# Kernel optimization log

Measured on AMD Instinct MI355X. Metric: run time of the kernel, lower is better.

Reference implementation:

```python
import jax, jax.numpy as jnp
import numpy as np
from jax import lax

WSZ = 8          # window_size
PZ = 8           # pool_size
FILTER_RATE = 0.3


def _gelu(x):
    return jax.nn.gelu(x, approximate=False)  # torch nn.GELU default = exact erf


def setup_inputs() -> dict:
    key = jax.random.key(0)
    ks = jax.random.split(key, 10)
    B, C, H, W = 2, 128, 512, 512
    feature_map = jax.random.normal(ks[0], (B, C, H, W), dtype=jnp.float32)
    uncertain_map = jax.random.uniform(ks[1], (B, H, W), dtype=jnp.float32)
    s = 0.02
    return {
        "feature_map": feature_map,
        "uncertain_map": uncertain_map,
        "q_g_w": jax.random.normal(ks[2], (C, C), dtype=jnp.float32) * s,
        "kv_g_w": jax.random.normal(ks[3], (2 * C, C), dtype=jnp.float32) * s,
        "linner0_w": jax.random.normal(ks[4], (C, C), dtype=jnp.float32) * s,
        "linner0_b": jnp.zeros((C,), dtype=jnp.float32),
        "qkv0_w": jax.random.normal(ks[5], (3 * C, C), dtype=jnp.float32) * s,
        "proj_w": jax.random.normal(ks[6], (C, C), dtype=jnp.float32) * s,
        "proj_b": jnp.zeros((C,), dtype=jnp.float32),
    }


def _forward(feature_map, uncertain_map, q_g_w, kv_g_w, linner0_w, linner0_b,
             qkv0_w, proj_w, proj_b):
    B, C, H, W = feature_map.shape
    wsz, pz = WSZ, PZ
    winsz = wsz * wsz
    nH, nW = H // wsz, W // wsz
    nWin = nH * nW
    scale = (C) ** (-0.5)  # num_heads = 1

    # --- window partition (shift_direct = No_Shift: no padding) ---
    # win_unc: (B, nWin, winsz)
    win_unc = uncertain_map.reshape(B, nH, wsz, nW, wsz).swapaxes(2, 3)
    win_unc = win_unc.reshape(B, nWin, winsz)
    # win_x: (B*nWin, winsz, C)
    win_x = feature_map.transpose(0, 2, 3, 1)  # B,H,W,C
    win_x = win_x.reshape(B, nH, wsz, nW, wsz, C).swapaxes(2, 3)
    win_x = win_x.reshape(B * nWin, winsz, C)

    # --- topk window selection + gather ---
    win_score = win_unc.mean(-1)                 # (B, nWin)
    nWF = int(nWin * FILTER_RATE)
    _, idx = lax.top_k(win_score, nWF)           # (B, nWF)
    flat_idx = (idx + jnp.arange(B, dtype=idx.dtype)[:, None] * nWin).reshape(-1)
    wf = win_x[flat_idx]                         # (B*nWF, winsz, C)

    # --- global branch ---
    # adaptive avg pool (H,W) -> (pz,pz): exact block mean since H%pz==0
    gx = feature_map.reshape(B, C, pz, H // pz, pz, W // pz).mean(axis=(3, 5))
    q = (wf @ q_g_w.T).reshape(B, nWF * winsz, C)
    g = gx.reshape(B, C, pz * pz).swapaxes(1, 2)          # (B, pz*pz, C)
    kv = (g @ kv_g_w.T).reshape(B, pz * pz, 2, C)
    k, v = kv[:, :, 0], kv[:, :, 1]
    attn = jax.nn.softmax(jnp.einsum('bqc,bkc->bqk', q, k) * scale, axis=-1)
    wf = wf + jnp.einsum('bqk,bkc->bqc', attn, v).reshape(B * nWF, winsz, C)

    # --- local branch (local_repeat = 1) ---
    wf = wf + _gelu(wf @ linner0_w.T + linner0_b)
    qkv = (wf @ qkv0_w.T).reshape(B * nWF, winsz, 3, C)
    q, k, v = qkv[:, :, 0], qkv[:, :, 1], qkv[:, :, 2]
    attn = jax.nn.softmax(jnp.einsum('nqc,nkc->nqk', q, k) * scale, axis=-1)
    av = jnp.einsum('nqk,nkc->nqc', attn, v)
    # faithful to torch: (attn@v).transpose(1,2).reshape(n, winsz, C)
    wf = wf + jnp.swapaxes(av, 1, 2).reshape(B * nWF, winsz, C)

    # --- proj ---
    wf = wf + _gelu(wf @ proj_w.T + proj_b)

    # --- scatter back + window merge ---
    win_x = win_x.at[flat_idx].set(wf)
    out = win_x.reshape(B, nH, nW, wsz, wsz, C).swapaxes(2, 3)
    out = out.reshape(B, H, W, C).transpose(0, 3, 1, 2)   # B,C,H,W
    return out


def reference(feature_map, uncertain_map, q_g_w, kv_g_w, linner0_w, linner0_b,
              qkv0_w, proj_w, proj_b):
    return _forward(feature_map, uncertain_map, q_g_w, kv_g_w, linner0_w,
                    linner0_b, qkv0_w, proj_w, proj_b)
```

## Files before the change

kernel.cpp:

```cpp
#include <hip/hip_runtime.h>
#include <math.h>

#define B_    2
#define C_    128
#define H_    512
#define W_    512
#define NWIN  4096
#define NWF   1228
#define NSEL  (B_*NWF)
#define SCALE 0.08838834764831845f

#define WFS   132

__device__ __forceinline__ float wave_max64(float v){
  #pragma unroll
  for (int off = 32; off; off >>= 1) v = fmaxf(v, __shfl_xor(v, off, 64));
  return v;
}
__device__ __forceinline__ float wave_sum64(float v){
  #pragma unroll
  for (int off = 32; off; off >>= 1) v += __shfl_xor(v, off, 64);
  return v;
}
__device__ __forceinline__ float gelu_f(float x){
  return 0.5f * x * (1.0f + erff(x * 0.70710678118654752440f));
}

__global__ void score_k(const float* __restrict__ unc, float* __restrict__ scores){
  int win = blockIdx.x;
  int b = win >> 12, w12 = win & 4095;
  int ih = w12 >> 6, iw = w12 & 63;
  int t = threadIdx.x, r = t >> 3, s = t & 7;
  float v = unc[((size_t)b*512 + ih*8 + r)*512 + iw*8 + s];
  v = wave_sum64(v);
  if (t == 0) scores[win] = v * (1.0f/64.0f);
}

__global__ void select_k(const float* __restrict__ scores, int* __restrict__ sel){
  int b = blockIdx.x;
  __shared__ float s[NWIN];
  for (int i = threadIdx.x; i < NWIN; i += 1024) s[i] = scores[b*NWIN + i];
  __syncthreads();
  for (int w = threadIdx.x; w < NWIN; w += 1024){
    float mys = s[w];
    int rank = 0;
    for (int j2 = 0; j2 < NWIN; ++j2){
      float o = s[j2];
      rank += (o > mys) || (o == mys && j2 < w);
    }
    if (rank < NWF) sel[b*NWF + rank] = w;
  }
}

__global__ void pool_k(const float* __restrict__ fm, float* __restrict__ g){
  int id = blockIdx.x;
  int p = id & 63, c = (id >> 6) & 127, b = id >> 13;
  int i = p >> 3, k = p & 7;
  const float* base = fm + (((size_t)b*128 + c)*512 + i*64)*512 + k*64;
  int tid = threadIdx.x;
  float sum = 0.0f;
  #pragma unroll
  for (int it = 0; it < 16; ++it){
    int f = it*256 + tid;
    int j2 = f >> 6, l = f & 63;
    sum += base[(size_t)j2*512 + l];
  }
  __shared__ float red[256];
  red[tid] = sum; __syncthreads();
  for (int s2 = 128; s2; s2 >>= 1){
    if (tid < s2) red[tid] += red[tid + s2];
    __syncthreads();
  }
  if (tid == 0) g[((b*64 + p) << 7) + c] = red[0] * (1.0f/4096.0f);
}

__global__ void kv_k(const float* __restrict__ g, const float* __restrict__ kvw,
                     float* __restrict__ kbuf, float* __restrict__ vbp){
  int gid = blockIdx.x*256 + threadIdx.x;
  int c = gid & 127, p = (gid >> 7) & 63, b = gid >> 13;
  const float* grow = g + ((b*64 + p) << 7);
  const float* wk = kvw + (c << 7);
  const float* wv = kvw + ((128 + c) << 7);
  float ka = 0.0f, va = 0.0f;
  #pragma unroll 8
  for (int d = 0; d < 128; ++d){ float gv = grow[d]; ka += gv*wk[d]; va += gv*wv[d]; }
  kbuf[gid] = ka;
  vbp[((((b*16 + (p >> 2))*128 + c)) << 2) + (p & 3)] = va;
}

__global__ void mb_k(const float* __restrict__ kbuf, const float* __restrict__ qgw,
                     float* __restrict__ mbp){
  int gid = blockIdx.x*256 + threadIdx.x;
  int d = gid & 127, p = (gid >> 7) & 63, b = gid >> 13;
  const float* krow = kbuf + ((b*64 + p) << 7);
  float acc = 0.0f;
  #pragma unroll 8
  for (int c = 0; c < 128; ++c) acc += krow[c] * qgw[(c << 7) + d];
  mbp[((((b*32 + (d >> 2))*64 + p)) << 2) + (d & 3)] = acc;
}

__global__ void m2p_k(const float* __restrict__ qkvw, float* __restrict__ m2p){
  int gid = blockIdx.x*256 + threadIdx.x;
  int e = gid & 127, dq = gid >> 7;
  float ax = 0.f, ay = 0.f, az = 0.f, aw = 0.f;
  for (int c = 0; c < 128; ++c){
    float kv2 = qkvw[((128 + c) << 7) + e];
    const float4 q4 = *(const float4*)(qkvw + (c << 7) + dq*4);
    ax += q4.x*kv2; ay += q4.y*kv2; az += q4.z*kv2; aw += q4.w*kv2;
  }
  ((float4*)m2p)[dq*128 + e] = make_float4(ax, ay, az, aw);
}

__global__ void pack_k(const float* __restrict__ l0w, const float* __restrict__ pw,
                       const float* __restrict__ qkvw,
                       float* __restrict__ l0wp, float* __restrict__ pwp,
                       float* __restrict__ wv2p){
  int gid = blockIdx.x*256 + threadIdx.x;
  int c = gid & 127, dq = gid >> 7;
  ((float4*)l0wp)[dq*128 + c] = *(const float4*)(l0w + (c << 7) + dq*4);
  ((float4*)pwp )[dq*128 + c] = *(const float4*)(pw  + (c << 7) + dq*4);
  ((float4*)wv2p)[dq*128 + c] = *(const float4*)(qkvw + ((256 + c) << 7) + dq*4);
}

__global__ __launch_bounds__(256, 2) void mega_k(
    const float* __restrict__ fm, const int* __restrict__ sel,
    const float* __restrict__ mbp, const float* __restrict__ vbp,
    const float* __restrict__ m2p, const float* __restrict__ wv2p,
    const float* __restrict__ l0wp, const float* __restrict__ l0b,
    const float* __restrict__ pwp,  const float* __restrict__ pb,
    float* __restrict__ out)
{
  __shared__ float wf_s[64*WFS];
  __shared__ float aux_s[64*128];
  const int tid = threadIdx.x, lane = tid & 63, wv = tid >> 6;
  const int ci = tid & 127, hi = tid >> 7;
  const int j = blockIdx.x;
  const int b = j / NWF;
  const int win = sel[j];
  const int ih = win >> 6, iw = win & 63;

  {
    const float* fmb = fm + ((size_t)b*128)*512*512;
    #pragma unroll
    for (int it = 0; it < 8; ++it){
      int idx = it*256 + tid;
      int c = idx >> 4, rem = idx & 15, r = rem >> 1, q = rem & 1;
      float4 v = *(const float4*)(fmb + ((size_t)c*512 + ih*8 + r)*512 + iw*8 + q*4);
      int t0 = r*8 + q*4;
      wf_s[(t0+0)*WFS + c] = v.x;
      wf_s[(t0+1)*WFS + c] = v.y;
      wf_s[(t0+2)*WFS + c] = v.z;
      wf_s[(t0+3)*WFS + c] = v.w;
    }
  }
  __syncthreads();

  {
    const float4* mb4 = (const float4*)mbp + (size_t)b*2048 + lane;
    float acc[16];
    #pragma unroll
    for (int r2 = 0; r2 < 16; ++r2) acc[r2] = 0.f;
    const float* wrow = wf_s + (wv*16)*WFS;
    float4 m = mb4[0];
    for (int dq = 0; dq < 32; ++dq){
      int nq = (dq + 1 < 32) ? dq + 1 : 31;
      float4 mn = mb4[nq*64];
      #pragma unroll
      for (int r2 = 0; r2 < 16; ++r2){
        float4 x = *(const float4*)(wrow + r2*WFS + dq*4);
        acc[r2] += x.x*m.x + x.y*m.y + x.z*m.z + x.w*m.w;
      }
      m = mn;
    }
    #pragma unroll
    for (int r2 = 0; r2 < 16; ++r2){
      float a = acc[r2] * SCALE;
      float mx = wave_max64(a);
      float e = __expf(a - mx);
      float p = e / wave_sum64(e);
      aux_s[(wv*16 + r2)*128 + lane] = p;
    }
  }
  __syncthreads();

  {
    const float4* v4p = (const float4*)vbp + (size_t)b*2048 + ci;
    float acc[32];
    #pragma unroll
    for (int jj = 0; jj < 32; ++jj) acc[jj] = 0.f;
    float4 v = v4p[0];
    for (int pq = 0; pq < 16; ++pq){
      int nq = (pq + 1 < 16) ? pq + 1 : 15;
      float4 vn = v4p[nq*128];
      #pragma unroll
      for (int jj = 0; jj < 32; ++jj){
        float4 p4 = *(const float4*)(aux_s + (2*jj + hi)*128 + pq*4);
        acc[jj] += p4.x*v.x + p4.y*v.y + p4.z*v.z + p4.w*v.w;
      }
      v = vn;
    }
    #pragma unroll
    for (int jj = 0; jj < 32; ++jj) wf_s[(2*jj + hi)*WFS + ci] += acc[jj];
  }
  __syncthreads();

  {
    const float4* w4 = (const float4*)l0wp + ci;
    float bias = l0b[ci];
    float acc[32];
    #pragma unroll
    for (int jj = 0; jj < 32; ++jj) acc[jj] = bias;
    float4 w = w4[0];
    for (int dq = 0; dq < 32; ++dq){
      int nq = (dq + 1 < 32) ? dq + 1 : 31;
      float4 wn = w4[nq*128];
      #pragma unroll
      for (int jj = 0; jj < 32; ++jj){
        float4 x = *(const float4*)(wf_s + (2*jj + hi)*WFS + dq*4);
        acc[jj] += x.x*w.x + x.y*w.y + x.z*w.z + x.w*w.w;
      }
      w = wn;
    }
    __syncthreads();
    #pragma unroll
    for (int jj = 0; jj < 32; ++jj)
      wf_s[(2*jj + hi)*WFS + ci] += gelu_f(acc[jj]);
  }
  __syncthreads();

  {
    const float4* w4 = (const float4*)m2p + ci;
    float acc[32];
    #pragma unroll
    for (int jj = 0; jj < 32; ++jj) acc[jj] = 0.f;
    float4 w = w4[0];
    for (int dq = 0; dq < 32; ++dq){
      int nq = (dq + 1 < 32) ? dq + 1 : 31;
      float4 wn = w4[nq*128];
      #pragma unroll
      for (int jj = 0; jj < 32; ++jj){
        float4 x = *(const float4*)(wf_s + (2*jj + hi)*WFS + dq*4);
        acc[jj] += x.x*w.x + x.y*w.y + x.z*w.z + x.w*w.w;
      }
      w = wn;
    }
    #pragma unroll
    for (int jj = 0; jj < 32; ++jj) aux_s[(2*jj + hi)*128 + ci] = acc[jj];
  }
  __syncthreads();

  {
    float acc[16];
    #pragma unroll
    for (int r2 = 0; r2 < 16; ++r2) acc[r2] = 0.f;
    const float* trow = aux_s + (wv*16)*128;
    for (int eq = 0; eq < 32; ++eq){
      float4 wr = *(const float4*)(wf_s + lane*WFS + eq*4);
      #pragma unroll
      for (int r2 = 0; r2 < 16; ++r2){
        float4 t4 = *(const float4*)(trow + r2*128 + eq*4);
        acc[r2] += t4.x*wr.x + t4.y*wr.y + t4.z*wr.z + t4.w*wr.w;
      }
    }
    #pragma unroll
    for (int r2 = 0; r2 < 16; ++r2){
      float a = acc[r2] * SCALE;
      float mx = wave_max64(a);
      float e = __expf(a - mx);
      float p = e / wave_sum64(e);
      aux_s[(wv*16 + r2)*128 + lane] = p;
    }
  }
  __syncthreads();

  {
    float acc[32];
    #pragma unroll
    for (int jj = 0; jj < 32; ++jj) acc[jj] = 0.f;
    for (int tq = 0; tq < 16; ++tq){
      float w0 = wf_s[(4*tq + 0)*WFS + ci];
      float w1 = wf_s[(4*tq + 1)*WFS + ci];
      float w2 = wf_s[(4*tq + 2)*WFS + ci];
      float w3 = wf_s[(4*tq + 3)*WFS + ci];
      #pragma unroll
      for (int jj = 0; jj < 32; ++jj){
        float4 p4 = *(const float4*)(aux_s + (2*jj + hi)*128 + tq*4);
        acc[jj] += p4.x*w0 + p4.y*w1 + p4.z*w2 + p4.w*w3;
      }
    }
    __syncthreads();
    #pragma unroll
    for (int jj = 0; jj < 32; ++jj) aux_s[(2*jj + hi)*128 + ci] = acc[jj];
  }
  __syncthreads();

  {
    const float4* w4 = (const float4*)wv2p + ci;
    float acc[32];
    #pragma unroll
    for (int jj = 0; jj < 32; ++jj) acc[jj] = 0.f;
    float4 w = w4[0];
    for (int dq = 0; dq < 32; ++dq){
      int nq = (dq + 1 < 32) ? dq + 1 : 31;
      float4 wn = w4[nq*128];
      #pragma unroll
      for (int jj = 0; jj < 32; ++jj){
        float4 u4 = *(const float4*)(aux_s + (2*jj + hi)*128 + dq*4);
        acc[jj] += u4.x*w.x + u4.y*w.y + u4.z*w.z + u4.w*w.w;
      }
      w = wn;
    }
    int row = ci >> 1, cbase = (ci & 1)*64 + hi;
    #pragma unroll
    for (int jj = 0; jj < 32; ++jj)
      wf_s[row*WFS + cbase + 2*jj] += acc[jj];
  }
  __syncthreads();

  {
    const float4* w4 = (const float4*)pwp + ci;
    float bias = pb[ci];
    float acc[32];
    #pragma unroll
    for (int jj = 0; jj < 32; ++jj) acc[jj] = bias;
    float4 w = w4[0];
    for (int dq = 0; dq < 32; ++dq){
      int nq = (dq + 1 < 32) ? dq + 1 : 31;
      float4 wn = w4[nq*128];
      #pragma unroll
      for (int jj = 0; jj < 32; ++jj){
        float4 x = *(const float4*)(wf_s + (2*jj + hi)*WFS + dq*4);
        acc[jj] += x.x*w.x + x.y*w.y + x.z*w.z + x.w*w.w;
      }
      w = wn;
    }
    __syncthreads();
    #pragma unroll
    for (int jj = 0; jj < 32; ++jj)
      wf_s[(2*jj + hi)*WFS + ci] += gelu_f(acc[jj]);
  }
  __syncthreads();

  {
    float* outb = out + ((size_t)b*128)*512*512;
    #pragma unroll
    for (int it = 0; it < 8; ++it){
      int idx = it*256 + tid;
      int c = idx >> 4, rem = idx & 15, r = rem >> 1, q = rem & 1;
      int t0 = r*8 + q*4;
      float4 v;
      v.x = wf_s[(t0+0)*WFS + c];
      v.y = wf_s[(t0+1)*WFS + c];
      v.z = wf_s[(t0+2)*WFS + c];
      v.w = wf_s[(t0+3)*WFS + c];
      *(float4*)(outb + ((size_t)c*512 + ih*8 + r)*512 + iw*8 + q*4) = v;
    }
  }
}

extern "C" void kernel_launch(void* const* d_in, const int* in_sizes, int n_in,
                              void* d_out, int out_size, void* d_ws, size_t ws_size,
                              hipStream_t stream) {
  const float* fm   = (const float*)d_in[0];
  const float* unc  = (const float*)d_in[1];
  const float* qgw  = (const float*)d_in[2];
  const float* kvw  = (const float*)d_in[3];
  const float* l0w  = (const float*)d_in[4];
  const float* l0b  = (const float*)d_in[5];
  const float* qkvw = (const float*)d_in[6];
  const float* pw   = (const float*)d_in[7];
  const float* pb   = (const float*)d_in[8];
  float* out = (float*)d_out;

  float* ws     = (float*)d_ws;
  float* scores = ws;
  int*   sel    = (int*)(ws + 8192);
  float* g      = ws + 12288;
  float* mbp    = ws + 12288;
  float* kbuf   = ws + 28672;
  float* wv2p   = ws + 28672;
  float* vbp    = ws + 45056;
  float* m2p    = ws + 61440;
  float* l0wp   = ws + 77824;
  float* pwp    = ws + 94208;

  hipMemcpyAsync(out, fm, (size_t)B_*C_*H_*W_*sizeof(float),
                 hipMemcpyDeviceToDevice, stream);

  score_k <<<B_*NWIN, 64, 0, stream>>>(unc, scores);
  select_k<<<B_, 1024, 0, stream>>>(scores, sel);
  pool_k  <<<B_*C_*64, 256, 0, stream>>>(fm, g);
  kv_k    <<<64, 256, 0, stream>>>(g, kvw, kbuf, vbp);
  mb_k    <<<64, 256, 0, stream>>>(kbuf, qgw, mbp);
  m2p_k   <<<16, 256, 0, stream>>>(qkvw, m2p);
  pack_k  <<<16, 256, 0, stream>>>(l0w, pw, qkvw, l0wp, pwp, wv2p);
  mega_k  <<<NSEL, 256, 0, stream>>>(fm, sel, mbp, vbp, m2p, wv2p,
                                     l0wp, l0b, pwp, pb, out);
}
```

Baseline: 2.069 ms.

## Fuse output copy into pool kernel and remap mega_k to row-per-wave work

The separate device-to-device copy of the feature map into the output is removed, and pool_k now writes each float4 it reads to the output, so the 268MB tensor is read once instead of twice. In mega_k each wave now owns 16 token rows and computes both 64-column halves, so several stages only depend on rows the wave itself produced and most __syncthreads barriers are dropped. Accumulations are split into sequential per-element adds. The risks are higher register pressure from the two 16-wide accumulator sets and correctness depending on the reduced barriers being sufficient.

```diff
diff --git a/kernel.cpp b/kernel.cpp
--- a/kernel.cpp
+++ b/kernel.cpp
@@ -52,18 +52,23 @@
   }
 }
 
-__global__ void pool_k(const float* __restrict__ fm, float* __restrict__ g){
+__global__ void pool_k(const float* __restrict__ fm, float* __restrict__ g,
+                       float* __restrict__ out){
   int id = blockIdx.x;
   int p = id & 63, c = (id >> 6) & 127, b = id >> 13;
   int i = p >> 3, k = p & 7;
-  const float* base = fm + (((size_t)b*128 + c)*512 + i*64)*512 + k*64;
+  size_t off = (((size_t)b*128 + c)*512 + i*64)*512 + k*64;
+  const float* base = fm + off;
+  float* ob = out + off;
   int tid = threadIdx.x;
   float sum = 0.0f;
   #pragma unroll
-  for (int it = 0; it < 16; ++it){
-    int f = it*256 + tid;
-    int j2 = f >> 6, l = f & 63;
-    sum += base[(size_t)j2*512 + l];
+  for (int it = 0; it < 4; ++it){
+    int idx = it*256 + tid;
+    int j2 = idx >> 4, l = (idx & 15)*4;
+    float4 v = *(const float4*)(base + (size_t)j2*512 + l);
+    *(float4*)(ob + (size_t)j2*512 + l) = v;
+    sum += v.x + v.y + v.z + v.w;
   }
   __shared__ float red[256];
   red[tid] = sum; __syncthreads();
@@ -133,7 +138,7 @@
   __shared__ float wf_s[64*WFS];
   __shared__ float aux_s[64*128];
   const int tid = threadIdx.x, lane = tid & 63, wv = tid >> 6;
-  const int ci = tid & 127, hi = tid >> 7;
+  const int r0 = wv*16;
   const int j = blockIdx.x;
   const int b = j / NWF;
   const int win = sel[j];
@@ -159,185 +164,204 @@
     const float4* mb4 = (const float4*)mbp + (size_t)b*2048 + lane;
     float acc[16];
     #pragma unroll
-    for (int r2 = 0; r2 < 16; ++r2) acc[r2] = 0.f;
-    const float* wrow = wf_s + (wv*16)*WFS;
+    for (int k = 0; k < 16; ++k) acc[k] = 0.f;
+    const float* wrow = wf_s + r0*WFS;
     float4 m = mb4[0];
     for (int dq = 0; dq < 32; ++dq){
       int nq = (dq + 1 < 32) ? dq + 1 : 31;
       float4 mn = mb4[nq*64];
       #pragma unroll
-      for (int r2 = 0; r2 < 16; ++r2){
-        float4 x = *(const float4*)(wrow + r2*WFS + dq*4);
-        acc[r2] += x.x*m.x + x.y*m.y + x.z*m.z + x.w*m.w;
+      for (int k = 0; k < 16; ++k){
+        float4 x = *(const float4*)(wrow + k*WFS + dq*4);
+        acc[k] += x.x*m.x; acc[k] += x.y*m.y; acc[k] += x.z*m.z; acc[k] += x.w*m.w;
       }
       m = mn;
     }
     #pragma unroll
-    for (int r2 = 0; r2 < 16; ++r2){
-      float a = acc[r2] * SCALE;
+    for (int k = 0; k < 16; ++k){
+      float a = acc[k] * SCALE;
       float mx = wave_max64(a);
       float e = __expf(a - mx);
       float p = e / wave_sum64(e);
-      aux_s[(wv*16 + r2)*128 + lane] = p;
-    }
-  }
-  __syncthreads();
-
-  {
-    const float4* v4p = (const float4*)vbp + (size_t)b*2048 + ci;
-    float acc[32];
-    #pragma unroll
-    for (int jj = 0; jj < 32; ++jj) acc[jj] = 0.f;
-    float4 v = v4p[0];
+      aux_s[(r0 + k)*128 + lane] = p;
+    }
+  }
+
+  {
+    const float4* v4 = (const float4*)vbp + (size_t)b*2048 + lane;
+    float a0[16], a1[16];
+    #pragma unroll
+    for (int k = 0; k < 16; ++k){ a0[k] = 0.f; a1[k] = 0.f; }
+    float4 v0 = v4[0], v1 = v4[64];
     for (int pq = 0; pq < 16; ++pq){
       int nq = (pq + 1 < 16) ? pq + 1 : 15;
-      float4 vn = v4p[nq*128];
-      #pragma unroll
-      for (int jj = 0; jj < 32; ++jj){
-        float4 p4 = *(const float4*)(aux_s + (2*jj + hi)*128 + pq*4);
-        acc[jj] += p4.x*v.x + p4.y*v.y + p4.z*v.z + p4.w*v.w;
-      }
-      v = vn;
-    }
-    #pragma unroll
-    for (int jj = 0; jj < 32; ++jj) wf_s[(2*jj + hi)*WFS + ci] += acc[jj];
-  }
-  __syncthreads();
-
-  {
-    const float4* w4 = (const float4*)l0wp + ci;
-    float bias = l0b[ci];
-    float acc[32];
-    #pragma unroll
-    for (int jj = 0; jj < 32; ++jj) acc[jj] = bias;
-    float4 w = w4[0];
+      float4 v0n = v4[nq*128], v1n = v4[nq*128 + 64];
+      #pragma unroll
+      for (int k = 0; k < 16; ++k){
+        float4 p4 = *(const float4*)(aux_s + (r0 + k)*128 + pq*4);
+        a0[k] += p4.x*v0.x; a0[k] += p4.y*v0.y; a0[k] += p4.z*v0.z; a0[k] += p4.w*v0.w;
+        a1[k] += p4.x*v1.x; a1[k] += p4.y*v1.y; a1[k] += p4.z*v1.z; a1[k] += p4.w*v1.w;
+      }
+      v0 = v0n; v1 = v1n;
+    }
+    #pragma unroll
+    for (int k = 0; k < 16; ++k){
+      wf_s[(r0 + k)*WFS + lane]      += a0[k];
+      wf_s[(r0 + k)*WFS + lane + 64] += a1[k];
+    }
+  }
+
+  {
+    const float4* w4 = (const float4*)l0wp + lane;
+    float bias0 = l0b[lane], bias1 = l0b[lane + 64];
+    float a0[16], a1[16];
+    #pragma unroll
+    for (int k = 0; k < 16; ++k){ a0[k] = bias0; a1[k] = bias1; }
+    float4 w0 = w4[0], w1 = w4[64];
     for (int dq = 0; dq < 32; ++dq){
       int nq = (dq + 1 < 32) ? dq + 1 : 31;
-      float4 wn = w4[nq*128];
-      #pragma unroll
-      for (int jj = 0; jj < 32; ++jj){
-        float4 x = *(const float4*)(wf_s + (2*jj + hi)*WFS + dq*4);
-        acc[jj] += x.x*w.x + x.y*w.y + x.z*w.z + x.w*w.w;
-      }
-      w = wn;
-    }
-    __syncthreads();
-    #pragma unroll
-    for (int jj = 0; jj < 32; ++jj)
-      wf_s[(2*jj + hi)*WFS + ci] += gelu_f(acc[jj]);
-  }
-  __syncthreads();
-
-  {
-    const float4* w4 = (const float4*)m2p + ci;
-    float acc[32];
-    #pragma unroll
-    for (int jj = 0; jj < 32; ++jj) acc[jj] = 0.f;
-    float4 w = w4[0];
+      float4 w0n = w4[nq*128], w1n = w4[nq*128 + 64];
+      #pragma unroll
+      for (int k = 0; k < 16; ++k){
+        float4 x = *(const float4*)(wf_s + (r0 + k)*WFS + dq*4);
+        a0[k] += x.x*w0.x; a0[k] += x.y*w0.y; a0[k] += x.z*w0.z; a0[k] += x.w*w0.w;
+        a1[k] += x.x*w1.x; a1[k] += x.y*w1.y; a1[k] += x.z*w1.z; a1[k] += x.w*w1.w;
+      }
+      w0 = w0n; w1 = w1n;
+    }
+    #pragma unroll
+    for (int k = 0; k < 16; ++k){
+      wf_s[(r0 + k)*WFS + lane]      += gelu_f(a0[k]);
+      wf_s[(r0 + k)*WFS + lane + 64] += gelu_f(a1[k]);
+    }
+  }
+
+  {
+    const float4* w4 = (const float4*)m2p + lane;
+    float a0[16], a1[16];
+    #pragma unroll
+    for (int k = 0; k < 16; ++k){ a0[k] = 0.f; a1[k] = 0.f; }
+    float4 w0 = w4[0], w1 = w4[64];
     for (int dq = 0; dq < 32; ++dq){
       int nq = (dq + 1 < 32) ? dq + 1 : 31;
-      float4 wn = w4[nq*128];
-      #pragma unroll
-      for (int jj = 0; jj < 32; ++jj){
-        float4 x = *(const float4*)(wf_s + (2*jj + hi)*WFS + dq*4);
-        acc[jj] += x.x*w.x + x.y*w.y + x.z*w.z + x.w*w.w;
-      }
-      w = wn;
-    }
-    #pragma unroll
-    for (int jj = 0; jj < 32; ++jj) aux_s[(2*jj + hi)*128 + ci] = acc[jj];
+      float4 w0n = w4[nq*128], w1n = w4[nq*128 + 64];
+      #pragma unroll
+      for (int k = 0; k < 16; ++k){
+        float4 x = *(const float4*)(wf_s + (r0 + k)*WFS + dq*4);
+        a0[k] += x.x*w0.x; a0[k] += x.y*w0.y; a0[k] += x.z*w0.z; a0[k] += x.w*w0.w;
+        a1[k] += x.x*w1.x; a1[k] += x.y*w1.y; a1[k] += x.z*w1.z; a1[k] += x.w*w1.w;
+      }
+      w0 = w0n; w1 = w1n;
+    }
+    #pragma unroll
+    for (int k = 0; k < 16; ++k){
+      aux_s[(r0 + k)*128 + lane]      = a0[k];
+      aux_s[(r0 + k)*128 + lane + 64] = a1[k];
+    }
   }
   __syncthreads();
 
   {
     float acc[16];
     #pragma unroll
-    for (int r2 = 0; r2 < 16; ++r2) acc[r2] = 0.f;
-    const float* trow = aux_s + (wv*16)*128;
+    for (int k = 0; k < 16; ++k) acc[k] = 0.f;
+    const float* trow = aux_s + r0*128;
     for (int eq = 0; eq < 32; ++eq){
       float4 wr = *(const float4*)(wf_s + lane*WFS + eq*4);
       #pragma unroll
-      for (int r2 = 0; r2 < 16; ++r2){
-        float4 t4 = *(const float4*)(trow + r2*128 + eq*4);
-        acc[r2] += t4.x*wr.x + t4.y*wr.y + t4.z*wr.z + t4.w*wr.w;
-      }
-    }
-    #pragma unroll
-    for (int r2 = 0; r2 < 16; ++r2){
-      float a = acc[r2] * SCALE;
+      for (int k = 0; k < 16; ++k){
+        float4 t4 = *(const float4*)(trow + k*128 + eq*4);
+        acc[k] += t4.x*wr.x; acc[k] += t4.y*wr.y; acc[k] += t4.z*wr.z; acc[k] += t4.w*wr.w;
+      }
+    }
+    #pragma unroll
+    for (int k = 0; k < 16; ++k){
+      float a = acc[k] * SCALE;
       float mx = wave_max64(a);
       float e = __expf(a - mx);
       float p = e / wave_sum64(e);
-      aux_s[(wv*16 + r2)*128 + lane] = p;
-    }
-  }
-  __syncthreads();
-
-  {
-    float acc[32];
-    #pragma unroll
-    for (int jj = 0; jj < 32; ++jj) acc[jj] = 0.f;
+      aux_s[(r0 + k)*128 + lane] = p;
+    }
+  }
+
+  {
+    float a0[16], a1[16];
+    #pragma unroll
+    for (int k = 0; k < 16; ++k){ a0[k] = 0.f; a1[k] = 0.f; }
     for (int tq = 0; tq < 16; ++tq){
-      float w0 = wf_s[(4*tq + 0)*WFS + ci];
-      float w1 = wf_s[(4*tq + 1)*WFS + ci];
-      float w2 = wf_s[(4*tq + 2)*WFS + ci];
-      float w3 = wf_s[(4*tq + 3)*WFS + ci];
-      #pragma unroll
-      for (int jj = 0; jj < 32; ++jj){
-        float4 p4 = *(const float4*)(aux_s + (2*jj + hi)*128 + tq*4);
-        acc[jj] += p4.x*w0 + p4.y*w1 + p4.z*w2 + p4.w*w3;
-      }
-    }
-    __syncthreads();
-    #pragma unroll
-    for (int jj = 0; jj < 32; ++jj) aux_s[(2*jj + hi)*128 + ci] = acc[jj];
-  }
-  __syncthreads();
-
-  {
-    const float4* w4 = (const float4*)wv2p + ci;
-    float acc[32];
-    #pragma unroll
-    for (int jj = 0; jj < 32; ++jj) acc[jj] = 0.f;
-    float4 w = w4[0];
+      float w00 = wf_s[(4*tq + 0)*WFS + lane];
+      float w01 = wf_s[(4*tq + 1)*WFS + lane];
+      float w02 = wf_s[(4*tq + 2)*WFS + lane];
+      float w03 = wf_s[(4*tq + 3)*WFS + lane];
+      float w10 = wf_s[(4*tq + 0)*WFS + lane + 64];
+      float w11 = wf_s[(4*tq + 1)*WFS + lane + 64];
+      float w12 = wf_s[(4*tq + 2)*WFS + lane + 64];
+      float w13 = wf_s[(4*tq + 3)*WFS + lane + 64];
+      #pragma unroll
+      for (int k = 0; k < 16; ++k){
+        float4 p4 = *(const float4*)(aux_s + (r0 + k)*128 + tq*4);
+        a0[k] += p4.x*w00; a0[k] += p4.y*w01; a0[k] += p4.z*w02; a0[k] += p4.w*w03;
+        a1[k] += p4.x*w10; a1[k] += p4.y*w11; a1[k] += p4.z*w12; a1[k] += p4.w*w13;
+      }
+    }
+    #pragma unroll
+    for (int k = 0; k < 16; ++k){
+      aux_s[(r0 + k)*128 + lane]      = a0[k];
+      aux_s[(r0 + k)*128 + lane + 64] = a1[k];
+    }
+  }
+
+  {
+    const float4* w4 = (const float4*)wv2p + lane;
+    float a0[16], a1[16];
+    #pragma unroll
+    for (int k = 0; k < 16; ++k){ a0[k] = 0.f; a1[k] = 0.f; }
+    float4 w0 = w4[0], w1 = w4[64];
     for (int dq = 0; dq < 32; ++dq){
       int nq = (dq + 1 < 32) ? dq + 1 : 31;
-      float4 wn = w4[nq*128];
-      #pragma unroll
-      for (int jj = 0; jj < 32; ++jj){
-        float4 u4 = *(const float4*)(aux_s + (2*jj + hi)*128 + dq*4);
-        acc[jj] += u4.x*w.x + u4.y*w.y + u4.z*w.z + u4.w*w.w;
-      }
-      w = wn;
-    }
-    int row = ci >> 1, cbase = (ci & 1)*64 + hi;
-    #pragma unroll
-    for (int jj = 0; jj < 32; ++jj)
-      wf_s[row*WFS + cbase + 2*jj] += acc[jj];
+      float4 w0n = w4[nq*128], w1n = w4[nq*128 + 64];
+      #pragma unroll
+      for (int k = 0; k < 16; ++k){
+        float4 u4 = *(const float4*)(aux_s + (r0 + k)*128 + dq*4);
+        a0[k] += u4.x*w0.x; a0[k] += u4.y*w0.y; a0[k] += u4.z*w0.z; a0[k] += u4.w*w0.w;
+        a1[k] += u4.x*w1.x; a1[k] += u4.y*w1.y; a1[k] += u4.z*w1.z; a1[k] += u4.w*w1.w;
+      }
+      w0 = w0n; w1 = w1n;
+    }
+    __syncthreads();
+    int rr = lane >> 1, cb = (lane & 1)*64;
+    #pragma unroll
+    for (int k = 0; k < 16; ++k){
+      int q = r0 + k;
+      wf_s[rr*WFS + cb + q]        += a0[k];
+      wf_s[(32 + rr)*WFS + cb + q] += a1[k];
+    }
   }
   __syncthreads();
 
   {
-    const float4* w4 = (const float4*)pwp + ci;
-    float bias = pb[ci];
-    float acc[32];
-    #pragma unroll
-    for (int jj = 0; jj < 32; ++jj) acc[jj] = bias;
-    float4 w = w4[0];
+    const float4* w4 = (const float4*)pwp + lane;
+    float bias0 = pb[lane], bias1 = pb[lane + 64];
+    float a0[16], a1[16];
+    #pragma unroll
+    for (int k = 0; k < 16; ++k){ a0[k] = bias0; a1[k] = bias1; }
+    float4 w0 = w4[0], w1 = w4[64];
     for (int dq = 0; dq < 32; ++dq){
       int nq = (dq + 1 < 32) ? dq + 1 : 31;
-      float4 wn = w4[nq*128];
-      #pragma unroll
-      for (int jj = 0; jj < 32; ++jj){
-        float4 x = *(const float4*)(wf_s + (2*jj + hi)*WFS + dq*4);
-        acc[jj] += x.x*w.x + x.y*w.y + x.z*w.z + x.w*w.w;
-      }
-      w = wn;
-    }
-    __syncthreads();
-    #pragma unroll
-    for (int jj = 0; jj < 32; ++jj)
-      wf_s[(2*jj + hi)*WFS + ci] += gelu_f(acc[jj]);
+      float4 w0n = w4[nq*128], w1n = w4[nq*128 + 64];
+      #pragma unroll
+      for (int k = 0; k < 16; ++k){
+        float4 x = *(const float4*)(wf_s + (r0 + k)*WFS + dq*4);
+        a0[k] += x.x*w0.x; a0[k] += x.y*w0.y; a0[k] += x.z*w0.z; a0[k] += x.w*w0.w;
+        a1[k] += x.x*w1.x; a1[k] += x.y*w1.y; a1[k] += x.z*w1.z; a1[k] += x.w*w1.w;
+      }
+      w0 = w0n; w1 = w1n;
+    }
+    #pragma unroll
+    for (int k = 0; k < 16; ++k){
+      wf_s[(r0 + k)*WFS + lane]      += gelu_f(a0[k]);
+      wf_s[(r0 + k)*WFS + lane + 64] += gelu_f(a1[k]);
+    }
   }
   __syncthreads();
 
@@ -384,12 +408,9 @@
   float* l0wp   = ws + 77824;
   float* pwp    = ws + 94208;
 
-  hipMemcpyAsync(out, fm, (size_t)B_*C_*H_*W_*sizeof(float),
-                 hipMemcpyDeviceToDevice, stream);
-
   score_k <<<B_*NWIN, 64, 0, stream>>>(unc, scores);
   select_k<<<B_, 1024, 0, stream>>>(scores, sel);
-  pool_k  <<<B_*C_*64, 256, 0, stream>>>(fm, g);
+  pool_k  <<<B_*C_*64, 256, 0, stream>>>(fm, g, out);
   kv_k    <<<64, 256, 0, stream>>>(g, kvw, kbuf, vbp);
   mb_k    <<<64, 256, 0, stream>>>(kbuf, qgw, mbp);
   m2p_k   <<<16, 256, 0, stream>>>(qkvw, m2p);
```

Measured after the change: 1.860 ms. 10.1% less time.
